# Kernel tuning notes

Measured on AMD Instinct MI355X. Metric: run time of the kernel, lower is better.

## Reference

```python
import jax, jax.numpy as jnp
import numpy as np

B, S, NN = 16, 512, 8          # batch, spatial nodes, neighbors per node
IN, H, NHEAD = 128, 512, 4     # input_size, hidden_size, n_head


def _forward(inputs, h, c, h_spatial, a_src, w_fg, b_fg, w_ig, b_ig,
             w_ih, w_hh, b_ih, b_hh):
    N = B * S
    x = inputs.reshape(N, IN)
    h = h.reshape(N, H)
    c = c.reshape(N, H)
    hs = h_spatial.reshape(N, NN, H)

    # attention logits: concat(h, neighbor) @ a_src, split to avoid materializing concat
    a_self, a_nb = a_src[:H], a_src[H:]              # [H, NHEAD] each
    attn = h @ a_self                                  # [N, NHEAD]
    attn = attn[:, None, :] + jnp.einsum('nkh,hm->nkm', hs, a_nb)  # [N, NN, NHEAD]
    attn = jnp.where(attn >= 0, attn, 0.2 * attn)      # leaky_relu(0.2)
    attn = jax.nn.softmax(attn, axis=1)                # softmax over neighbors

    # aggregate neighbors per head -> [N, NHEAD*H]
    agg = jnp.einsum('nkm,nkh->nmh', attn, hs).reshape(N, NHEAD * H)

    spatial_f = jax.nn.sigmoid(agg @ w_fg.T + b_fg)    # [N, H]
    spatial_i = jax.nn.sigmoid(agg @ w_ig.T + b_ig)
    h = h * spatial_i
    c = c * spatial_f

    # torch LSTMCell: gate order i, f, g, o
    gates = x @ w_ih.T + b_ih + h @ w_hh.T + b_hh      # [N, 4H]
    i_g, f_g, g_g, o_g = jnp.split(gates, 4, axis=1)
    i_g = jax.nn.sigmoid(i_g)
    f_g = jax.nn.sigmoid(f_g)
    g_g = jnp.tanh(g_g)
    o_g = jax.nn.sigmoid(o_g)
    c_new = f_g * c + i_g * g_g
    h_new = o_g * jnp.tanh(c_new)
    return h_new.reshape(B, S, H), c_new.reshape(B, S, H)


def setup_inputs() -> dict:
    key = jax.random.key(0)
    ks = jax.random.split(key, 16)
    xav = lambda k, shp: jax.random.uniform(
        k, shp, jnp.float32, -1.0, 1.0) * np.sqrt(6.0 / (shp[0] + shp[1]))
    return {
        'inputs': jax.random.normal(ks[0], (B, S, IN), jnp.float32),
        'h': jax.random.normal(ks[1], (B, S, H), jnp.float32),
        'c': jax.random.normal(ks[2], (B, S, H), jnp.float32),
        'h_spatial': jax.random.normal(ks[3], (B, S, NN, H), jnp.float32),
        'a_src': xav(ks[4], (2 * H, NHEAD)),
        'w_fg': jax.random.normal(ks[5], (H, NHEAD * H), jnp.float32) * 0.02,
        'b_fg': jnp.zeros((H,), jnp.float32),
        'w_ig': jax.random.normal(ks[6], (H, NHEAD * H), jnp.float32) * 0.02,
        'b_ig': jnp.zeros((H,), jnp.float32),
        'w_ih': jax.random.normal(ks[7], (4 * H, IN), jnp.float32) * 0.02,
        'w_hh': jax.random.normal(ks[8], (4 * H, H), jnp.float32) * 0.02,
        'b_ih': jnp.zeros((4 * H,), jnp.float32),
        'b_hh': jnp.zeros((4 * H,), jnp.float32),
    }


def reference(inputs, h, c, h_spatial, a_src, w_fg, b_fg, w_ig, b_ig,
              w_ih, w_hh, b_ih, b_hh):
    return _forward(inputs, h, c, h_spatial, a_src, w_fg, b_fg, w_ig, b_ig,
                    w_ih, w_hh, b_ih, b_hh)
```

## Files before the change

kernel.cpp:

```cpp
#include <hip/hip_runtime.h>
#include <hip/hip_bf16.h>
#include <cstdint>
#include <cstddef>

#define N_ROWS 8192
#define HDIM 512
#define INDIM 128
#define NHEADS 4
#define NNB 8

typedef __bf16 bf16_t;
typedef __bf16 bf16x8 __attribute__((ext_vector_type(8)));
typedef __bf16 bf16x4 __attribute__((ext_vector_type(4)));
typedef __bf16 bf16x2 __attribute__((ext_vector_type(2)));
typedef float f32x4 __attribute__((ext_vector_type(4)));

__device__ __forceinline__ float sigmoidf_(float x) { return 1.0f / (1.0f + expf(-x)); }

__device__ __forceinline__ void load_lds16(const void* g, void* l) {
  __builtin_amdgcn_global_load_lds(
      (const __attribute__((address_space(1))) void*)g,
      (__attribute__((address_space(3))) void*)l, 16, 0, 0);
}

__global__ __launch_bounds__(256) void pack_kernel(
    const float* __restrict__ w_fg, const float* __restrict__ w_ig,
    const float* __restrict__ w_ih, const float* __restrict__ w_hh,
    const float* __restrict__ b_ih, const float* __restrict__ b_hh,
    const float* __restrict__ x,
    bf16_t* __restrict__ W1, bf16_t* __restrict__ W2i,
    float* __restrict__ b2, bf16_t* __restrict__ A2)
{
  int idx = blockIdx.x * 256 + threadIdx.x;
  if (idx < 1024 * 2048) {
    int r = idx >> 11, k = idx & 2047;
    float v = (r < 512) ? w_fg[(size_t)r * 2048 + k] : w_ig[(size_t)(r - 512) * 2048 + k];
    W1[idx] = (bf16_t)v;
    return;
  }
  idx -= 1024 * 2048;
  if (idx < 2048 * 640) {
    int r = idx / 640, k = idx - r * 640;
    int rp = (r & 511) * 4 + (r >> 9);
    float v = (k < 128) ? w_ih[(size_t)r * 128 + k] : w_hh[(size_t)r * 512 + (k - 128)];
    W2i[(size_t)rp * 640 + k] = (bf16_t)v;
    return;
  }
  idx -= 2048 * 640;
  if (idx < 2048) {
    int q = idx >> 2, g = idx & 3;
    b2[idx] = b_ih[g * 512 + q] + b_hh[g * 512 + q];
    return;
  }
  idx -= 2048;
  if (idx < N_ROWS * INDIM) {
    int n = idx >> 7, cc = idx & 127;
    A2[(size_t)n * 640 + cc] = (bf16_t)x[idx];
  }
}

__global__ __launch_bounds__(256) void attn_agg_kernel(
    const float* __restrict__ h, const float* __restrict__ hs,
    const float* __restrict__ a_src, bf16_t* __restrict__ agg)
{
  __shared__ float s_hs[NNB][HDIM];
  __shared__ float s_h[HDIM];
  __shared__ float s_logit[NNB][NHEADS];
  __shared__ float s_self[NHEADS];

  const int n = blockIdx.x;
  const int t = threadIdx.x;
  const float* hs_n = hs + (size_t)n * (NNB * HDIM);
  const float* h_n  = h  + (size_t)n * HDIM;

  {
    const float4* s4 = (const float4*)hs_n;
    float4* d4 = (float4*)&s_hs[0][0];
#pragma unroll
    for (int i = 0; i < 4; ++i) d4[t + i * 256] = s4[t + i * 256];
    if (t < HDIM / 4) ((float4*)s_h)[t] = ((const float4*)h_n)[t];
  }
  __syncthreads();

  const int wave = t >> 6, lane = t & 63;
#pragma unroll
  for (int kk = 0; kk < 2; ++kk) {
    const int k = wave * 2 + kk;
    float acc0 = 0.f, acc1 = 0.f, acc2 = 0.f, acc3 = 0.f;
#pragma unroll
    for (int i = 0; i < HDIM / 64; ++i) {
      const int hh = i * 64 + lane;
      const float v = s_hs[k][hh];
      const float4 av = *(const float4*)(a_src + (size_t)(HDIM + hh) * NHEADS);
      acc0 += v * av.x; acc1 += v * av.y; acc2 += v * av.z; acc3 += v * av.w;
    }
    float accs[NHEADS] = {acc0, acc1, acc2, acc3};
#pragma unroll
    for (int m = 0; m < NHEADS; ++m) {
      float a = accs[m];
#pragma unroll
      for (int off = 32; off > 0; off >>= 1) a += __shfl_xor(a, off);
      if (lane == 0) s_logit[k][m] = a;
    }
  }
  if (wave == 0) {
    float acc0 = 0.f, acc1 = 0.f, acc2 = 0.f, acc3 = 0.f;
#pragma unroll
    for (int i = 0; i < HDIM / 64; ++i) {
      const int hh = i * 64 + lane;
      const float v = s_h[hh];
      const float4 av = *(const float4*)(a_src + (size_t)hh * NHEADS);
      acc0 += v * av.x; acc1 += v * av.y; acc2 += v * av.z; acc3 += v * av.w;
    }
    float accs[NHEADS] = {acc0, acc1, acc2, acc3};
#pragma unroll
    for (int m = 0; m < NHEADS; ++m) {
      float a = accs[m];
#pragma unroll
      for (int off = 32; off > 0; off >>= 1) a += __shfl_xor(a, off);
      if (lane == 0) s_self[m] = a;
    }
  }
  __syncthreads();

  float w[NNB][NHEADS];
#pragma unroll
  for (int m = 0; m < NHEADS; ++m) {
    const float sm = s_self[m];
    float mx = -1e30f;
#pragma unroll
    for (int k = 0; k < NNB; ++k) {
      float l = sm + s_logit[k][m];
      l = (l >= 0.f) ? l : 0.2f * l;
      w[k][m] = l;
      mx = fmaxf(mx, l);
    }
    float sum = 0.f;
#pragma unroll
    for (int k = 0; k < NNB; ++k) { const float e = expf(w[k][m] - mx); w[k][m] = e; sum += e; }
    const float inv = 1.f / sum;
#pragma unroll
    for (int k = 0; k < NNB; ++k) w[k][m] *= inv;
  }

  bf16_t* agg_n = agg + (size_t)n * (NHEADS * HDIM);
  const int hh = t * 2;
  float e0[NNB], e1[NNB];
#pragma unroll
  for (int k = 0; k < NNB; ++k) { e0[k] = s_hs[k][hh]; e1[k] = s_hs[k][hh + 1]; }
#pragma unroll
  for (int m = 0; m < NHEADS; ++m) {
    float a0 = 0.f, a1 = 0.f;
#pragma unroll
    for (int k = 0; k < NNB; ++k) { a0 += w[k][m] * e0[k]; a1 += w[k][m] * e1[k]; }
    bf16x2 pk; pk[0] = (bf16_t)a0; pk[1] = (bf16_t)a1;
    *(bf16x2*)(agg_n + m * HDIM + hh) = pk;
  }
}

__global__ __launch_bounds__(256) void gemm1_kernel(
    const bf16_t* __restrict__ A, const bf16_t* __restrict__ Bt,
    const float* __restrict__ b_fg, const float* __restrict__ b_ig,
    const float* __restrict__ c_in, const float* __restrict__ h_in,
    float* __restrict__ cprime, bf16_t* __restrict__ A2)
{
  __shared__ bf16_t At[128][32];
  __shared__ bf16_t Bs[64][32];

  const int tid  = threadIdx.x;
  const int wave = tid >> 6, lane = tid & 63;
  const int wr = wave >> 1, wc = wave & 1;
  const int bm0 = blockIdx.x * 128;
  const int bn0 = blockIdx.y * 64;
  const int K = 2048;

  f32x4 acc[4][2] = {};

  const int srow = tid >> 2;
  const int sch  = tid & 3;
  const int gsw8 = (sch ^ ((srow >> 1) & 3)) * 8;
  const int sch8 = sch * 8;
  const int frow = lane & 15;
  const int fro8 = ((lane >> 4) ^ ((frow >> 1) & 3)) * 8;

  for (int k0 = 0; k0 < K; k0 += 32) {
    load_lds16(A  + (size_t)(bm0 + srow)      * K + k0 + gsw8, &At[srow][sch8]);
    load_lds16(A  + (size_t)(bm0 + 64 + srow) * K + k0 + gsw8, &At[64 + srow][sch8]);
    load_lds16(Bt + (size_t)(bn0 + srow)      * K + k0 + gsw8, &Bs[srow][sch8]);
    __syncthreads();

    bf16x8 af[4], bv[2];
#pragma unroll
    for (int i = 0; i < 4; ++i) af[i] = *(const bf16x8*)&At[wr * 64 + i * 16 + frow][fro8];
#pragma unroll
    for (int j = 0; j < 2; ++j) bv[j] = *(const bf16x8*)&Bs[wc * 32 + j * 16 + frow][fro8];
#pragma unroll
    for (int i = 0; i < 4; ++i)
#pragma unroll
      for (int j = 0; j < 2; ++j)
        acc[i][j] = __builtin_amdgcn_mfma_f32_16x16x32_bf16(af[i], bv[j], acc[i][j], 0, 0, 0);
    __syncthreads();
  }

  const int col_in = lane & 15;
  const int row_in = (lane >> 4) * 4;
#pragma unroll
  for (int i = 0; i < 4; ++i) {
#pragma unroll
    for (int j = 0; j < 2; ++j) {
      const int col = bn0 + wc * 32 + j * 16 + col_in;
#pragma unroll
      for (int r = 0; r < 4; ++r) {
        const int row = bm0 + wr * 64 + i * 16 + row_in + r;
        const float v = acc[i][j][r];
        if (col < 512) {
          const float s = sigmoidf_(v + b_fg[col]);
          cprime[(size_t)row * 512 + col] = c_in[(size_t)row * 512 + col] * s;
        } else {
          const int jj = col - 512;
          const float s = sigmoidf_(v + b_ig[jj]);
          A2[(size_t)row * 640 + 128 + jj] = (bf16_t)(h_in[(size_t)row * 512 + jj] * s);
        }
      }
    }
  }
}

__global__ __launch_bounds__(256) void gemm2_kernel(
    const bf16_t* __restrict__ A, const bf16_t* __restrict__ Bt,
    const float* __restrict__ b2, const float* __restrict__ cprime,
    float* __restrict__ out)
{
  __shared__ union {
    struct { bf16_t A[128][32]; bf16_t B[128][32]; } st;
    float epi[64][128];
  } sm;

  const int tid  = threadIdx.x;
  const int wave = tid >> 6, lane = tid & 63;
  const int wr = wave >> 1, wc = wave & 1;
  const int bm0 = blockIdx.x * 128;
  const int bn0 = blockIdx.y * 128;
  const int K = 640;

  f32x4 acc[4][4] = {};

  const int srow = tid >> 2;
  const int sch  = tid & 3;
  const int gsw8 = (sch ^ ((srow >> 1) & 3)) * 8;
  const int sch8 = sch * 8;
  const int frow = lane & 15;
  const int fro8 = ((lane >> 4) ^ ((frow >> 1) & 3)) * 8;

  for (int k0 = 0; k0 < K; k0 += 32) {
    load_lds16(A  + (size_t)(bm0 + srow)      * K + k0 + gsw8, &sm.st.A[srow][sch8]);
    load_lds16(A  + (size_t)(bm0 + 64 + srow) * K + k0 + gsw8, &sm.st.A[64 + srow][sch8]);
    load_lds16(Bt + (size_t)(bn0 + srow)      * K + k0 + gsw8, &sm.st.B[srow][sch8]);
    load_lds16(Bt + (size_t)(bn0 + 64 + srow) * K + k0 + gsw8, &sm.st.B[64 + srow][sch8]);
    __syncthreads();

    bf16x8 af[4], bv[4];
#pragma unroll
    for (int i = 0; i < 4; ++i) af[i] = *(const bf16x8*)&sm.st.A[wr * 64 + i * 16 + frow][fro8];
#pragma unroll
    for (int j = 0; j < 4; ++j) bv[j] = *(const bf16x8*)&sm.st.B[wc * 64 + j * 16 + frow][fro8];
#pragma unroll
    for (int i = 0; i < 4; ++i)
#pragma unroll
      for (int j = 0; j < 4; ++j)
        acc[i][j] = __builtin_amdgcn_mfma_f32_16x16x32_bf16(af[i], bv[j], acc[i][j], 0, 0, 0);
    __syncthreads();
  }

  const int col_in = lane & 15;
  const int row_in = (lane >> 4) * 4;
  const int q0i = bn0 >> 2;
  const int qi  = tid & 31;
  const int r0  = tid >> 5;

#pragma unroll
  for (int p = 0; p < 2; ++p) {
    if (wr == p) {
#pragma unroll
      for (int i = 0; i < 4; ++i)
#pragma unroll
        for (int j = 0; j < 4; ++j)
#pragma unroll
          for (int r = 0; r < 4; ++r)
            sm.epi[i * 16 + row_in + r][wc * 64 + j * 16 + col_in] = acc[i][j][r];
    }
    __syncthreads();
    const float4 bb = *(const float4*)&b2[(size_t)(q0i + qi) * 4];
#pragma unroll
    for (int rr = 0; rr < 8; ++rr) {
      const int lr = r0 + rr * 8;
      const float4 g4 = *(const float4*)&sm.epi[lr][qi * 4];
      const int grow = bm0 + p * 64 + lr;
      const int q    = q0i + qi;
      const float cp = cprime[(size_t)grow * 512 + q];
      const float ig = sigmoidf_(g4.x + bb.x);
      const float fg = sigmoidf_(g4.y + bb.y);
      const float gg = tanhf(g4.z + bb.z);
      const float og = sigmoidf_(g4.w + bb.w);
      const float cn = fg * cp + ig * gg;
      const float hn = og * tanhf(cn);
      out[(size_t)grow * 512 + q] = hn;
      out[(size_t)N_ROWS * 512 + (size_t)grow * 512 + q] = cn;
    }
    __syncthreads();
  }
}

extern "C" void kernel_launch(void* const* d_in, const int* in_sizes, int n_in,
                              void* d_out, int out_size, void* d_ws, size_t ws_size,
                              hipStream_t stream) {
  const float* x     = (const float*)d_in[0];
  const float* h     = (const float*)d_in[1];
  const float* c     = (const float*)d_in[2];
  const float* hsp   = (const float*)d_in[3];
  const float* a_src = (const float*)d_in[4];
  const float* w_fg  = (const float*)d_in[5];
  const float* b_fg  = (const float*)d_in[6];
  const float* w_ig  = (const float*)d_in[7];
  const float* b_ig  = (const float*)d_in[8];
  const float* w_ih  = (const float*)d_in[9];
  const float* w_hh  = (const float*)d_in[10];
  const float* b_ih  = (const float*)d_in[11];
  const float* b_hh  = (const float*)d_in[12];
  float* out = (float*)d_out;

  uint8_t* ws = (uint8_t*)d_ws;
  bf16_t* agg    = (bf16_t*)(ws);
  bf16_t* W1     = (bf16_t*)(ws + 33554432);
  bf16_t* W2i    = (bf16_t*)(ws + 37748736);
  float*  b2     = (float*) (ws + 40370176);
  bf16_t* A2     = (bf16_t*)(ws + 40378368);
  float*  cprime = (float*) (ws + 50864128);

  pack_kernel<<<17416, 256, 0, stream>>>(w_fg, w_ig, w_ih, w_hh, b_ih, b_hh, x,
                                         W1, W2i, b2, A2);
  attn_agg_kernel<<<N_ROWS, 256, 0, stream>>>(h, hsp, a_src, agg);
  gemm1_kernel<<<dim3(64, 16), 256, 0, stream>>>(
      agg, W1, b_fg, b_ig, c, h, cprime, A2);
  gemm2_kernel<<<dim3(64, 16), 256, 0, stream>>>(
      A2, W2i, b2, cprime, out);
}
```

Measured before the change: 193.4 us.

## Deepen GEMM K-tile to 64 with 8-way swizzle and vectorize pack kernel

Both GEMM kernels now stage 64-wide K slices in LDS instead of 32, with a new 8-chunk XOR swizzle, and run two MFMA sub-steps per barrier pair. This halves the number of syncthreads and load phases per K, at the cost of twice the LDS footprint per block. The pack kernel now converts four floats per thread using float4 loads and bf16x4 stores, which cuts the thread count and the number of memory instructions.

```diff
diff --git a/kernel.cpp b/kernel.cpp
--- a/kernel.cpp
+++ b/kernel.cpp
@@ -32,30 +32,38 @@
     float* __restrict__ b2, bf16_t* __restrict__ A2)
 {
   int idx = blockIdx.x * 256 + threadIdx.x;
-  if (idx < 1024 * 2048) {
-    int r = idx >> 11, k = idx & 2047;
-    float v = (r < 512) ? w_fg[(size_t)r * 2048 + k] : w_ig[(size_t)(r - 512) * 2048 + k];
-    W1[idx] = (bf16_t)v;
+  if (idx < 524288) {
+    const int e = idx * 4, r = e >> 11, k = e & 2047;
+    const float* src = (r < 512) ? &w_fg[(size_t)r * 2048 + k]
+                                 : &w_ig[(size_t)(r - 512) * 2048 + k];
+    const float4 v = *(const float4*)src;
+    bf16x4 o; o[0] = (bf16_t)v.x; o[1] = (bf16_t)v.y; o[2] = (bf16_t)v.z; o[3] = (bf16_t)v.w;
+    *(bf16x4*)&W1[e] = o;
     return;
   }
-  idx -= 1024 * 2048;
-  if (idx < 2048 * 640) {
-    int r = idx / 640, k = idx - r * 640;
-    int rp = (r & 511) * 4 + (r >> 9);
-    float v = (k < 128) ? w_ih[(size_t)r * 128 + k] : w_hh[(size_t)r * 512 + (k - 128)];
-    W2i[(size_t)rp * 640 + k] = (bf16_t)v;
+  idx -= 524288;
+  if (idx < 327680) {
+    const int e = idx * 4, r = e / 640, k = e - r * 640;
+    const int rp = (r & 511) * 4 + (r >> 9);
+    const float* src = (k < 128) ? &w_ih[(size_t)r * 128 + k]
+                                 : &w_hh[(size_t)r * 512 + (k - 128)];
+    const float4 v = *(const float4*)src;
+    bf16x4 o; o[0] = (bf16_t)v.x; o[1] = (bf16_t)v.y; o[2] = (bf16_t)v.z; o[3] = (bf16_t)v.w;
+    *(bf16x4*)&W2i[(size_t)rp * 640 + k] = o;
     return;
   }
-  idx -= 2048 * 640;
+  idx -= 327680;
   if (idx < 2048) {
-    int q = idx >> 2, g = idx & 3;
+    const int q = idx >> 2, g = idx & 3;
     b2[idx] = b_ih[g * 512 + q] + b_hh[g * 512 + q];
     return;
   }
   idx -= 2048;
-  if (idx < N_ROWS * INDIM) {
-    int n = idx >> 7, cc = idx & 127;
-    A2[(size_t)n * 640 + cc] = (bf16_t)x[idx];
+  if (idx < 262144) {
+    const int e = idx * 4, n = e >> 7, cc = e & 127;
+    const float4 v = *(const float4*)&x[e];
+    bf16x4 o; o[0] = (bf16_t)v.x; o[1] = (bf16_t)v.y; o[2] = (bf16_t)v.z; o[3] = (bf16_t)v.w;
+    *(bf16x4*)&A2[(size_t)n * 640 + cc] = o;
   }
 }
 
@@ -164,8 +172,8 @@
     const float* __restrict__ c_in, const float* __restrict__ h_in,
     float* __restrict__ cprime, bf16_t* __restrict__ A2)
 {
-  __shared__ bf16_t At[128][32];
-  __shared__ bf16_t Bs[64][32];
+  __shared__ bf16_t At[128][64];
+  __shared__ bf16_t Bs[64][64];
 
   const int tid  = threadIdx.x;
   const int wave = tid >> 6, lane = tid & 63;
@@ -176,29 +184,40 @@
 
   f32x4 acc[4][2] = {};
 
-  const int srow = tid >> 2;
-  const int sch  = tid & 3;
-  const int gsw8 = (sch ^ ((srow >> 1) & 3)) * 8;
+  const int srow = tid >> 3;
+  const int sch  = tid & 7;
+  const int gsw8 = (sch ^ (srow & 7)) * 8;
   const int sch8 = sch * 8;
   const int frow = lane & 15;
-  const int fro8 = ((lane >> 4) ^ ((frow >> 1) & 3)) * 8;
-
-  for (int k0 = 0; k0 < K; k0 += 32) {
-    load_lds16(A  + (size_t)(bm0 + srow)      * K + k0 + gsw8, &At[srow][sch8]);
-    load_lds16(A  + (size_t)(bm0 + 64 + srow) * K + k0 + gsw8, &At[64 + srow][sch8]);
-    load_lds16(Bt + (size_t)(bn0 + srow)      * K + k0 + gsw8, &Bs[srow][sch8]);
-    __syncthreads();
-
-    bf16x8 af[4], bv[2];
-#pragma unroll
-    for (int i = 0; i < 4; ++i) af[i] = *(const bf16x8*)&At[wr * 64 + i * 16 + frow][fro8];
-#pragma unroll
-    for (int j = 0; j < 2; ++j) bv[j] = *(const bf16x8*)&Bs[wc * 32 + j * 16 + frow][fro8];
-#pragma unroll
-    for (int i = 0; i < 4; ++i)
+  const int fq   = lane >> 4;
+
+  for (int k0 = 0; k0 < K; k0 += 64) {
+#pragma unroll
+    for (int r = 0; r < 4; ++r)
+      load_lds16(A + (size_t)(bm0 + r * 32 + srow) * K + k0 + gsw8,
+                 &At[r * 32 + srow][sch8]);
+#pragma unroll
+    for (int r = 0; r < 2; ++r)
+      load_lds16(Bt + (size_t)(bn0 + r * 32 + srow) * K + k0 + gsw8,
+                 &Bs[r * 32 + srow][sch8]);
+    __syncthreads();
+
+#pragma unroll
+    for (int kk = 0; kk < 2; ++kk) {
+      const int fro8 = ((kk * 4 + fq) ^ (frow & 7)) * 8;
+      bf16x8 af[4], bv[2];
+#pragma unroll
+      for (int i = 0; i < 4; ++i)
+        af[i] = *(const bf16x8*)&At[wr * 64 + i * 16 + frow][fro8];
 #pragma unroll
       for (int j = 0; j < 2; ++j)
-        acc[i][j] = __builtin_amdgcn_mfma_f32_16x16x32_bf16(af[i], bv[j], acc[i][j], 0, 0, 0);
+        bv[j] = *(const bf16x8*)&Bs[wc * 32 + j * 16 + frow][fro8];
+#pragma unroll
+      for (int i = 0; i < 4; ++i)
+#pragma unroll
+        for (int j = 0; j < 2; ++j)
+          acc[i][j] = __builtin_amdgcn_mfma_f32_16x16x32_bf16(af[i], bv[j], acc[i][j], 0, 0, 0);
+    }
     __syncthreads();
   }
 
@@ -232,7 +251,7 @@
     float* __restrict__ out)
 {
   __shared__ union {
-    struct { bf16_t A[128][32]; bf16_t B[128][32]; } st;
+    struct { bf16_t A[128][64]; bf16_t B[128][64]; } st;
     float epi[64][128];
   } sm;
 
@@ -245,30 +264,40 @@
 
   f32x4 acc[4][4] = {};
 
-  const int srow = tid >> 2;
-  const int sch  = tid & 3;
-  const int gsw8 = (sch ^ ((srow >> 1) & 3)) * 8;
+  const int srow = tid >> 3;
+  const int sch  = tid & 7;
+  const int gsw8 = (sch ^ (srow & 7)) * 8;
   const int sch8 = sch * 8;
   const int frow = lane & 15;
-  const int fro8 = ((lane >> 4) ^ ((frow >> 1) & 3)) * 8;
-
-  for (int k0 = 0; k0 < K; k0 += 32) {
-    load_lds16(A  + (size_t)(bm0 + srow)      * K + k0 + gsw8, &sm.st.A[srow][sch8]);
-    load_lds16(A  + (size_t)(bm0 + 64 + srow) * K + k0 + gsw8, &sm.st.A[64 + srow][sch8]);
-    load_lds16(Bt + (size_t)(bn0 + srow)      * K + k0 + gsw8, &sm.st.B[srow][sch8]);
-    load_lds16(Bt + (size_t)(bn0 + 64 + srow) * K + k0 + gsw8, &sm.st.B[64 + srow][sch8]);
-    __syncthreads();
-
-    bf16x8 af[4], bv[4];
-#pragma unroll
-    for (int i = 0; i < 4; ++i) af[i] = *(const bf16x8*)&sm.st.A[wr * 64 + i * 16 + frow][fro8];
-#pragma unroll
-    for (int j = 0; j < 4; ++j) bv[j] = *(const bf16x8*)&sm.st.B[wc * 64 + j * 16 + frow][fro8];
-#pragma unroll
-    for (int i = 0; i < 4; ++i)
+  const int fq   = lane >> 4;
+
+  for (int k0 = 0; k0 < K; k0 += 64) {
+#pragma unroll
+    for (int r = 0; r < 4; ++r)
+      load_lds16(A + (size_t)(bm0 + r * 32 + srow) * K + k0 + gsw8,
+                 &sm.st.A[r * 32 + srow][sch8]);
+#pragma unroll
+    for (int r = 0; r < 4; ++r)
+      load_lds16(Bt + (size_t)(bn0 + r * 32 + srow) * K + k0 + gsw8,
+                 &sm.st.B[r * 32 + srow][sch8]);
+    __syncthreads();
+
+#pragma unroll
+    for (int kk = 0; kk < 2; ++kk) {
+      const int fro8 = ((kk * 4 + fq) ^ (frow & 7)) * 8;
+      bf16x8 af[4], bv[4];
+#pragma unroll
+      for (int i = 0; i < 4; ++i)
+        af[i] = *(const bf16x8*)&sm.st.A[wr * 64 + i * 16 + frow][fro8];
 #pragma unroll
       for (int j = 0; j < 4; ++j)
-        acc[i][j] = __builtin_amdgcn_mfma_f32_16x16x32_bf16(af[i], bv[j], acc[i][j], 0, 0, 0);
+        bv[j] = *(const bf16x8*)&sm.st.B[wc * 64 + j * 16 + frow][fro8];
+#pragma unroll
+      for (int i = 0; i < 4; ++i)
+#pragma unroll
+        for (int j = 0; j < 4; ++j)
+          acc[i][j] = __builtin_amdgcn_mfma_f32_16x16x32_bf16(af[i], bv[j], acc[i][j], 0, 0, 0);
+    }
     __syncthreads();
   }
 
@@ -337,8 +366,8 @@
   bf16_t* A2     = (bf16_t*)(ws + 40378368);
   float*  cprime = (float*) (ws + 50864128);
 
-  pack_kernel<<<17416, 256, 0, stream>>>(w_fg, w_ig, w_ih, w_hh, b_ih, b_hh, x,
-                                         W1, W2i, b2, A2);
+  pack_kernel<<<4360, 256, 0, stream>>>(w_fg, w_ig, w_ih, w_hh, b_ih, b_hh, x,
+                                        W1, W2i, b2, A2);
   attn_agg_kernel<<<N_ROWS, 256, 0, stream>>>(h, hsp, a_src, agg);
   gemm1_kernel<<<dim3(64, 16), 256, 0, stream>>>(
       agg, W1, b_fg, b_ig, c, h, cprime, A2);
```

After: 186.2 us. -3.7%, faster.
